# Kernel optimization log

Hardware: AMD Instinct MI355X
Metric: run time of the kernel (lower is better)

## Reference

```python
import jax, jax.numpy as jnp
import numpy as np

B, SQ, SK, D, H, DH = 4, 1024, 1024, 1024, 16, 64  # transform_units*head_units == 1024


def setup_inputs() -> dict:
    key = jax.random.key(0)
    ks = jax.random.split(key, 8)
    q = jax.random.normal(ks[0], (B, SQ, D), dtype=jnp.float32)
    v = jax.random.normal(ks[1], (B, SK, D), dtype=jnp.float32)
    q_mask = jax.random.randint(ks[2], (B, SQ), 0, 2).astype(bool).at[:, 0].set(True)
    v_mask = jax.random.randint(ks[3], (B, SK), 0, 2).astype(bool).at[:, 0].set(True)
    s = 0.02
    Wq = jax.random.normal(ks[4], (D, H * DH), dtype=jnp.float32) * s
    Wk = jax.random.normal(ks[5], (D, H * DH), dtype=jnp.float32) * s
    Wv = jax.random.normal(ks[6], (D, H * DH), dtype=jnp.float32) * s
    Wo = jax.random.normal(ks[7], (H * DH, D), dtype=jnp.float32) * s
    bq = jnp.zeros((H * DH,), jnp.float32)
    bk = jnp.zeros((H * DH,), jnp.float32)
    bv = jnp.zeros((H * DH,), jnp.float32)
    bo = jnp.zeros((D,), jnp.float32)
    return {"q": q, "v": v, "q_mask": q_mask, "v_mask": v_mask,
            "Wq": Wq, "bq": bq, "Wk": Wk, "bk": bk, "Wv": Wv, "bv": bv,
            "Wo": Wo, "bo": bo}


def reference(q, v, q_mask, v_mask, Wq, bq, Wk, bk, Wv, bv, Wo, bo):
    # k = v in the original module
    k = v
    # QKV projections; split-last-dim + batch-concat trick == reshape to heads
    Q = (q @ Wq + bq).reshape(B, SQ, H, DH)
    Kh = (k @ Wk + bk).reshape(B, SK, H, DH)
    V = (v @ Wv + bv).reshape(B, SK, H, DH)
    # Keras Attention: unscaled dot-product scores
    scores = jnp.einsum('bqhd,bkhd->bhqk', Q, Kh)  # [B,H,SQ,SK]
    scores = jnp.where(v_mask[:, None, None, :], scores, jnp.float32(-1e9))
    attn = jax.nn.softmax(scores, axis=-1)
    ctx = jnp.einsum('bhqk,bkhd->bqhd', attn, V).reshape(B, SQ, H * DH)
    # Keras Attention zeros masked query positions before output dense
    ctx = ctx * q_mask[:, :, None].astype(ctx.dtype)
    return ctx @ Wo + bo
```

## Files before the change

kernel.cpp:

```cpp
#include <hip/hip_runtime.h>
#include <hip/hip_fp16.h>

typedef __attribute__((ext_vector_type(8))) _Float16 f16x8;
typedef __attribute__((ext_vector_type(4))) float f32x4;

__device__ __forceinline__ void gload_lds16(const _Float16* g, _Float16* l) {
  __builtin_amdgcn_global_load_lds((const __attribute__((address_space(1))) void*)g,
                                   (__attribute__((address_space(3))) void*)l, 16, 0, 0);
}

__global__ __launch_bounds__(256) void cvt2_kernel(const float* __restrict__ q,
                                                   const float* __restrict__ v,
                                                   _Float16* __restrict__ q16,
                                                   _Float16* __restrict__ v16) {
  int i = blockIdx.x * 256 + threadIdx.x;
  const float* in = blockIdx.y ? v : q;
  _Float16* out = blockIdx.y ? v16 : q16;
  float4 f = ((const float4*)in)[i];
  union { _Float16 h[4]; uint2 u; } o;
  o.h[0] = (_Float16)f.x; o.h[1] = (_Float16)f.y;
  o.h[2] = (_Float16)f.z; o.h[3] = (_Float16)f.w;
  *(uint2*)&out[4 * i] = o.u;
}

__global__ __launch_bounds__(256) void transpose_cvt4_kernel(
    const float* __restrict__ W0, const float* __restrict__ W1,
    const float* __restrict__ W2, const float* __restrict__ W3,
    _Float16* __restrict__ T0, _Float16* __restrict__ T1,
    _Float16* __restrict__ T2, _Float16* __restrict__ T3) {
  int z = blockIdx.z;
  const float* W = (z == 0) ? W0 : (z == 1) ? W1 : (z == 2) ? W2 : W3;
  _Float16* T = (z == 0) ? T0 : (z == 1) ? T1 : (z == 2) ? T2 : T3;
  __shared__ float tile[64 * 65];
  int bx = blockIdx.x * 64, by = blockIdx.y * 64;
  int tid = threadIdx.x;
  for (int it = 0; it < 4; it++) {
    int lin = it * 256 + tid;
    int r = lin >> 4, q4 = (lin & 15) * 4;
    float4 f = *(const float4*)&W[(size_t)(by + r) * 1024 + bx + q4];
    tile[r * 65 + q4 + 0] = f.x;
    tile[r * 65 + q4 + 1] = f.y;
    tile[r * 65 + q4 + 2] = f.z;
    tile[r * 65 + q4 + 3] = f.w;
  }
  __syncthreads();
  for (int it = 0; it < 2; it++) {
    int lin = it * 256 + tid;
    int orow = lin >> 3, seg = (lin & 7) * 8;
    union { uint4 u; _Float16 h[8]; } o;
    for (int e = 0; e < 8; e++) o.h[e] = (_Float16)tile[(seg + e) * 65 + orow];
    *(uint4*)&T[(size_t)(bx + orow) * 1024 + by + seg] = o.u;
  }
}

__global__ __launch_bounds__(256) void transpose_v_kernel(const _Float16* __restrict__ V16,
                                                          _Float16* __restrict__ VT16) {
  __shared__ float tile[64 * 65];
  int kb = blockIdx.x, h = blockIdx.y, b = blockIdx.z;
  int tid = threadIdx.x;
  for (int it = 0; it < 2; it++) {
    int lin = it * 256 + tid;
    int r = lin >> 3, s8 = (lin & 7) * 8;
    union { uint4 u; _Float16 h[8]; } iv;
    iv.u = *(const uint4*)&V16[(size_t)(b * 1024 + kb * 64 + r) * 1024 + h * 64 + s8];
    for (int e = 0; e < 8; e++) tile[r * 65 + s8 + e] = (float)iv.h[e];
  }
  __syncthreads();
  for (int it = 0; it < 2; it++) {
    int lin = it * 256 + tid;
    int dh = lin >> 3, s8 = (lin & 7) * 8;
    union { uint4 u; _Float16 h[8]; } o;
    for (int e = 0; e < 8; e++) o.h[e] = (_Float16)tile[(s8 + e) * 65 + dh];
    *(uint4*)&VT16[((size_t)((b * 16 + h) * 64 + dh)) * 1024 + kb * 64 + s8] = o.u;
  }
}

__global__ __launch_bounds__(256) void gemm_qkv_kernel(
    const _Float16* __restrict__ q16, const _Float16* __restrict__ v16,
    const _Float16* __restrict__ WqT, const _Float16* __restrict__ WkT,
    const _Float16* __restrict__ WvT,
    const float* __restrict__ bq, const float* __restrict__ bk, const float* __restrict__ bv,
    _Float16* __restrict__ Q16, _Float16* __restrict__ K16, _Float16* __restrict__ V16) {
  int z = blockIdx.z;
  const _Float16* A = (z == 0) ? q16 : v16;
  const _Float16* BT = (z == 0) ? WqT : ((z == 1) ? WkT : WvT);
  const float* bias = (z == 0) ? bq : ((z == 1) ? bk : bv);
  _Float16* C = (z == 0) ? Q16 : ((z == 1) ? K16 : V16);
  int m0 = blockIdx.y * 128, n0 = blockIdx.x * 128;
  const int K = 1024, N = 1024;

  __shared__ _Float16 Alds[128 * 64];
  __shared__ _Float16 Blds[128 * 64];
  int tid = threadIdx.x, lane = tid & 63, w = tid >> 6;
  int c = lane & 15, g = lane >> 4;
  int wm = (w & 1) * 64, wn = (w >> 1) * 64;
  int lr = lane >> 3, ls = (lane & 7) * 8;

  const _Float16* ga[4]; const _Float16* gb[4];
  _Float16* la[4]; _Float16* lb[4];
  for (int p = 0; p < 4; p++) {
    int chunk = w * 4 + p;
    int row = chunk * 8 + lr;
    ga[p] = &A[(size_t)(m0 + row) * K + ls];
    gb[p] = &BT[(size_t)(n0 + row) * K + ls];
    la[p] = Alds + chunk * 512;
    lb[p] = Blds + chunk * 512;
  }

  f32x4 acc[4][4];
  for (int i = 0; i < 4; i++)
    for (int j = 0; j < 4; j++)
      acc[i][j] = (f32x4){0.f, 0.f, 0.f, 0.f};

  for (int kt = 0; kt < K; kt += 64) {
    __syncthreads();
    for (int p = 0; p < 4; p++) {
      gload_lds16(ga[p] + kt, la[p]);
      gload_lds16(gb[p] + kt, lb[p]);
    }
    __syncthreads();
    for (int ks = 0; ks < 2; ks++) {
      f16x8 af[4], bf[4];
      for (int i = 0; i < 4; i++)
        af[i] = *(const f16x8*)&Alds[(wm + i * 16 + c) * 64 + ks * 32 + g * 8];
      for (int j = 0; j < 4; j++)
        bf[j] = *(const f16x8*)&Blds[(wn + j * 16 + c) * 64 + ks * 32 + g * 8];
      for (int i = 0; i < 4; i++)
        for (int j = 0; j < 4; j++)
          acc[i][j] = __builtin_amdgcn_mfma_f32_16x16x32_f16(af[i], bf[j], acc[i][j], 0, 0, 0);
    }
  }
  for (int j = 0; j < 4; j++) {
    float bv_ = bias[n0 + wn + j * 16 + c];
    for (int i = 0; i < 4; i++) {
      int r = m0 + wm + i * 16 + g * 4;
      int cc = n0 + wn + j * 16 + c;
      for (int e = 0; e < 4; e++)
        C[(size_t)(r + e) * N + cc] = (_Float16)(acc[i][j][e] + bv_);
    }
  }
}

__global__ __launch_bounds__(256) void gemm_out_kernel(
    const _Float16* __restrict__ ctx16, const _Float16* __restrict__ WoT,
    const float* __restrict__ bo, float* __restrict__ out) {
  int m0 = blockIdx.y * 128, n0 = blockIdx.x * 64;
  const int K = 1024, N = 1024;
  __shared__ _Float16 Alds[128 * 64];
  __shared__ _Float16 Blds[64 * 64];
  int tid = threadIdx.x, lane = tid & 63, w = tid >> 6;
  int c = lane & 15, g = lane >> 4;
  int wm = (w & 1) * 64, wn = (w >> 1) * 32;
  int lr = lane >> 3, ls = (lane & 7) * 8;

  const _Float16* ga[4]; _Float16* la[4];
  const _Float16* gb[2]; _Float16* lb[2];
  for (int p = 0; p < 4; p++) {
    int chunk = w * 4 + p;
    int row = chunk * 8 + lr;
    ga[p] = &ctx16[(size_t)(m0 + row) * K + ls];
    la[p] = Alds + chunk * 512;
  }
  for (int p = 0; p < 2; p++) {
    int chunk = w * 2 + p;
    int row = chunk * 8 + lr;
    gb[p] = &WoT[(size_t)(n0 + row) * K + ls];
    lb[p] = Blds + chunk * 512;
  }

  f32x4 acc[4][2];
  for (int i = 0; i < 4; i++)
    for (int j = 0; j < 2; j++)
      acc[i][j] = (f32x4){0.f, 0.f, 0.f, 0.f};

  for (int kt = 0; kt < K; kt += 64) {
    __syncthreads();
    for (int p = 0; p < 4; p++) gload_lds16(ga[p] + kt, la[p]);
    for (int p = 0; p < 2; p++) gload_lds16(gb[p] + kt, lb[p]);
    __syncthreads();
    for (int ks = 0; ks < 2; ks++) {
      f16x8 af[4], bf[2];
      for (int i = 0; i < 4; i++)
        af[i] = *(const f16x8*)&Alds[(wm + i * 16 + c) * 64 + ks * 32 + g * 8];
      for (int j = 0; j < 2; j++)
        bf[j] = *(const f16x8*)&Blds[(wn + j * 16 + c) * 64 + ks * 32 + g * 8];
      for (int i = 0; i < 4; i++)
        for (int j = 0; j < 2; j++)
          acc[i][j] = __builtin_amdgcn_mfma_f32_16x16x32_f16(af[i], bf[j], acc[i][j], 0, 0, 0);
    }
  }
  for (int j = 0; j < 2; j++) {
    float bv_ = bo[n0 + wn + j * 16 + c];
    for (int i = 0; i < 4; i++) {
      int r = m0 + wm + i * 16 + g * 4;
      int cc = n0 + wn + j * 16 + c;
      for (int e = 0; e < 4; e++)
        out[(size_t)(r + e) * N + cc] = acc[i][j][e] + bv_;
    }
  }
}

__global__ __launch_bounds__(256, 4) void attn_kernel(
    const _Float16* __restrict__ Q16, const _Float16* __restrict__ K16,
    const _Float16* __restrict__ VT16,
    const int* __restrict__ q_mask, const int* __restrict__ v_mask,
    _Float16* __restrict__ ctx16) {
  int qb = blockIdx.x, h = blockIdx.y, b = blockIdx.z;
  int tid = threadIdx.x, lane = tid & 63, w = tid >> 6;
  int c = lane & 15, g = lane >> 4;
  int lr = lane >> 3, ls = lane & 7;

  __shared__ _Float16 QP[64 * 64];
  __shared__ _Float16 Kl[2][64 * 64];
  __shared__ _Float16 Vl[2][64 * 64];

  const _Float16* Qg = Q16 + ((size_t)(b * 1024 + qb * 64)) * 1024 + h * 64;
  const _Float16* Kg = K16 + ((size_t)(b * 1024)) * 1024 + h * 64;
  const _Float16* Vg = VT16 + ((size_t)(b * 16 + h)) * 64 * 1024;

  int row0 = w * 16 + lr, row1 = row0 + 8;
  int kx = (ls ^ lr) * 8;
  int ch0 = w * 2, ch1 = w * 2 + 1;

  gload_lds16(Qg + (size_t)row0 * 1024 + kx, QP + ch0 * 512);
  gload_lds16(Qg + (size_t)row1 * 1024 + kx, QP + ch1 * 512);
  gload_lds16(Kg + (size_t)row0 * 1024 + kx, &Kl[0][ch0 * 512]);
  gload_lds16(Kg + (size_t)row1 * 1024 + kx, &Kl[0][ch1 * 512]);
  gload_lds16(Vg + (size_t)row0 * 1024 + kx, &Vl[0][ch0 * 512]);
  gload_lds16(Vg + (size_t)row1 * 1024 + kx, &Vl[0][ch1 * 512]);
  __syncthreads();

  f16x8 qf[2];
  {
    int row = w * 16 + c;
    const char* rb = (const char*)QP + row * 128;
    int x = (row & 7) << 4;
    qf[0] = *(const f16x8*)(rb + ((g * 16) ^ x));
    qf[1] = *(const f16x8*)(rb + ((64 + g * 16) ^ x));
    const _Float16 l2e = (_Float16)1.44269504f;
    for (int e = 0; e < 8; e++) { qf[0][e] *= l2e; qf[1][e] *= l2e; }
  }

  float lp[4] = {0.f, 0.f, 0.f, 0.f};
  f32x4 acc_o[4];
  for (int jd = 0; jd < 4; jd++) acc_o[jd] = (f32x4){0.f, 0.f, 0.f, 0.f};

  char* pb = (char*)QP;
  int cur = 0;
  const float REF = -23.0831222f;
  for (int kb = 0; kb < 16; kb++) {
    if (kb + 1 < 16) {
      int nb = cur ^ 1;
      const _Float16* kgs = Kg + (size_t)(kb + 1) * 64 * 1024;
      const _Float16* vgs = Vg + (kb + 1) * 64;
      gload_lds16(kgs + (size_t)row0 * 1024 + kx, &Kl[nb][ch0 * 512]);
      gload_lds16(kgs + (size_t)row1 * 1024 + kx, &Kl[nb][ch1 * 512]);
      gload_lds16(vgs + (size_t)row0 * 1024 + kx, &Vl[nb][ch0 * 512]);
      gload_lds16(vgs + (size_t)row1 * 1024 + kx, &Vl[nb][ch1 * 512]);
    }
    float madd[4];
    for (int j = 0; j < 4; j++)
      madd[j] = v_mask[b * 1024 + kb * 64 + j * 16 + c] ? REF : -1e30f;

    f32x4 s[4];
    const char* kbse = (const char*)&Kl[cur][0];
    for (int j = 0; j < 4; j++) {
      int row = j * 16 + c;
      const char* rb = kbse + row * 128;
      int x = (row & 7) << 4;
      f16x8 k0 = *(const f16x8*)(rb + ((g * 16) ^ x));
      f16x8 k1 = *(const f16x8*)(rb + ((64 + g * 16) ^ x));
      s[j] = (f32x4){0.f, 0.f, 0.f, 0.f};
      s[j] = __builtin_amdgcn_mfma_f32_16x16x32_f16(qf[0], k0, s[j], 0, 0, 0);
      s[j] = __builtin_amdgcn_mfma_f32_16x16x32_f16(qf[1], k1, s[j], 0, 0, 0);
    }

    for (int j = 0; j < 4; j++)
      for (int e = 0; e < 4; e++) {
        float p = exp2f(s[j][e] + madd[j]);
        s[j][e] = p;
        lp[e] += p;
      }

    for (int j = 0; j < 4; j++)
      for (int e = 0; e < 4; e++) {
        int prow = w * 16 + g * 4 + e;
        int pby = prow * 128 + (((j * 16 + c) * 2) ^ ((prow & 7) << 4));
        *(_Float16*)(pb + pby) = (_Float16)s[j][e];
      }
    asm volatile("s_waitcnt lgkmcnt(0)" ::: "memory");
    __builtin_amdgcn_sched_barrier(0);

    const char* vbse = (const char*)&Vl[cur][0];
    for (int ks = 0; ks < 2; ks++) {
      int prow = w * 16 + c;
      f16x8 pf = *(const f16x8*)(pb + prow * 128 +
                                 ((ks * 64 + g * 16) ^ ((prow & 7) << 4)));
      for (int jd = 0; jd < 4; jd++) {
        int vrow = jd * 16 + c;
        f16x8 vf = *(const f16x8*)(vbse + vrow * 128 +
                                   ((ks * 64 + g * 16) ^ ((vrow & 7) << 4)));
        acc_o[jd] = __builtin_amdgcn_mfma_f32_16x16x32_f16(pf, vf, acc_o[jd], 0, 0, 0);
      }
    }

    __syncthreads();
    cur ^= 1;
  }

  for (int e = 0; e < 4; e++) {
    lp[e] += __shfl_xor(lp[e], 1);
    lp[e] += __shfl_xor(lp[e], 2);
    lp[e] += __shfl_xor(lp[e], 4);
    lp[e] += __shfl_xor(lp[e], 8);
  }

  int qrow = b * 1024 + qb * 64 + w * 16 + g * 4;
  float inv[4];
  for (int e = 0; e < 4; e++) {
    float qm = q_mask[qrow + e] ? 1.0f : 0.0f;
    inv[e] = qm / lp[e];
  }
  _Float16* cb = ctx16 + ((size_t)qrow) * 1024 + h * 64;
  for (int jd = 0; jd < 4; jd++)
    for (int e = 0; e < 4; e++)
      cb[(size_t)e * 1024 + jd * 16 + c] = (_Float16)(acc_o[jd][e] * inv[e]);
}

extern "C" void kernel_launch(void* const* d_in, const int* in_sizes, int n_in,
                              void* d_out, int out_size, void* d_ws, size_t ws_size,
                              hipStream_t stream) {
  const float* q  = (const float*)d_in[0];
  const float* v  = (const float*)d_in[1];
  const int* q_mask = (const int*)d_in[2];
  const int* v_mask = (const int*)d_in[3];
  const float* Wq = (const float*)d_in[4];
  const float* bq = (const float*)d_in[5];
  const float* Wk = (const float*)d_in[6];
  const float* bk = (const float*)d_in[7];
  const float* Wv = (const float*)d_in[8];
  const float* bv = (const float*)d_in[9];
  const float* Wo = (const float*)d_in[10];
  const float* bo = (const float*)d_in[11];
  float* out = (float*)d_out;

  _Float16* ws = (_Float16*)d_ws;
  const size_t NE = (size_t)4 * 1024 * 1024;
  _Float16* q16   = ws;
  _Float16* v16   = ws + NE;
  _Float16* Q16   = ws + 2 * NE;
  _Float16* K16   = ws + 3 * NE;
  _Float16* V16   = ws + 4 * NE;
  _Float16* ctx16 = ws + 5 * NE;
  _Float16* WqT   = ws + 6 * NE;
  _Float16* WkT   = WqT + 1024 * 1024;
  _Float16* WvT   = WkT + 1024 * 1024;
  _Float16* WoT   = WvT + 1024 * 1024;
  _Float16* VT16  = q16;

  cvt2_kernel<<<dim3(4096, 2), 256, 0, stream>>>(q, v, q16, v16);
  transpose_cvt4_kernel<<<dim3(16, 16, 4), 256, 0, stream>>>(Wq, Wk, Wv, Wo, WqT, WkT, WvT, WoT);
  gemm_qkv_kernel<<<dim3(8, 32, 3), 256, 0, stream>>>(q16, v16, WqT, WkT, WvT,
                                                      bq, bk, bv, Q16, K16, V16);
  transpose_v_kernel<<<dim3(16, 16, 4), 256, 0, stream>>>(V16, VT16);
  attn_kernel<<<dim3(16, 16, 4), 256, 0, stream>>>(Q16, K16, VT16, q_mask, v_mask, ctx16);
  gemm_out_kernel<<<dim3(16, 32), 256, 0, stream>>>(ctx16, WoT, bo, out);
}
```

Measured before the change: 224.3 us.

## Double-buffer GEMM LDS tiles with XOR swizzle, fuse prep and V transpose

Both GEMM kernels now double-buffer their LDS tiles. Each iteration prefetches the next K tile with global_load_lds while MFMAs run on the current one, with a single barrier per iteration. Loads and reads use an XOR swizzle on the 16-byte column chunk to cut LDS bank conflicts. The fp16 conversion and weight transpose kernels merge into one launch, and the V projection epilogue writes V transposed per head directly, removing the separate transpose kernel and its round trip through global memory. The costs are doubled LDS use, which may lower occupancy, and scattered 8-byte stores in the V epilogue.

Result: no change. 221.9 us (-1.0%).

```diff
diff --git a/kernel.cpp b/kernel.cpp
--- a/kernel.cpp
+++ b/kernel.cpp
@@ -9,31 +9,32 @@
                                    (__attribute__((address_space(3))) void*)l, 16, 0, 0);
 }
 
-__global__ __launch_bounds__(256) void cvt2_kernel(const float* __restrict__ q,
-                                                   const float* __restrict__ v,
-                                                   _Float16* __restrict__ q16,
-                                                   _Float16* __restrict__ v16) {
-  int i = blockIdx.x * 256 + threadIdx.x;
-  const float* in = blockIdx.y ? v : q;
-  _Float16* out = blockIdx.y ? v16 : q16;
-  float4 f = ((const float4*)in)[i];
-  union { _Float16 h[4]; uint2 u; } o;
-  o.h[0] = (_Float16)f.x; o.h[1] = (_Float16)f.y;
-  o.h[2] = (_Float16)f.z; o.h[3] = (_Float16)f.w;
-  *(uint2*)&out[4 * i] = o.u;
-}
-
-__global__ __launch_bounds__(256) void transpose_cvt4_kernel(
+__global__ __launch_bounds__(256) void prep_kernel(
+    const float* __restrict__ q, const float* __restrict__ v,
     const float* __restrict__ W0, const float* __restrict__ W1,
     const float* __restrict__ W2, const float* __restrict__ W3,
+    _Float16* __restrict__ q16, _Float16* __restrict__ v16,
     _Float16* __restrict__ T0, _Float16* __restrict__ T1,
     _Float16* __restrict__ T2, _Float16* __restrict__ T3) {
-  int z = blockIdx.z;
+  __shared__ float tile[64 * 65];
+  int tid = threadIdx.x, ybl = blockIdx.y;
+  if (ybl < 16) {
+    int i = (ybl * 256 + blockIdx.x) * 256 + tid;
+    float4 fq = ((const float4*)q)[i];
+    float4 fv = ((const float4*)v)[i];
+    union { _Float16 h[4]; uint2 u; } oq, ov;
+    oq.h[0] = (_Float16)fq.x; oq.h[1] = (_Float16)fq.y;
+    oq.h[2] = (_Float16)fq.z; oq.h[3] = (_Float16)fq.w;
+    ov.h[0] = (_Float16)fv.x; ov.h[1] = (_Float16)fv.y;
+    ov.h[2] = (_Float16)fv.z; ov.h[3] = (_Float16)fv.w;
+    *(uint2*)&q16[4 * (size_t)i] = oq.u;
+    *(uint2*)&v16[4 * (size_t)i] = ov.u;
+    return;
+  }
+  int z = ybl - 16;
   const float* W = (z == 0) ? W0 : (z == 1) ? W1 : (z == 2) ? W2 : W3;
   _Float16* T = (z == 0) ? T0 : (z == 1) ? T1 : (z == 2) ? T2 : T3;
-  __shared__ float tile[64 * 65];
-  int bx = blockIdx.x * 64, by = blockIdx.y * 64;
-  int tid = threadIdx.x;
+  int bx = (blockIdx.x & 15) * 64, by = (blockIdx.x >> 4) * 64;
   for (int it = 0; it < 4; it++) {
     int lin = it * 256 + tid;
     int r = lin >> 4, q4 = (lin & 15) * 4;
@@ -53,58 +54,35 @@
   }
 }
 
-__global__ __launch_bounds__(256) void transpose_v_kernel(const _Float16* __restrict__ V16,
-                                                          _Float16* __restrict__ VT16) {
-  __shared__ float tile[64 * 65];
-  int kb = blockIdx.x, h = blockIdx.y, b = blockIdx.z;
-  int tid = threadIdx.x;
-  for (int it = 0; it < 2; it++) {
-    int lin = it * 256 + tid;
-    int r = lin >> 3, s8 = (lin & 7) * 8;
-    union { uint4 u; _Float16 h[8]; } iv;
-    iv.u = *(const uint4*)&V16[(size_t)(b * 1024 + kb * 64 + r) * 1024 + h * 64 + s8];
-    for (int e = 0; e < 8; e++) tile[r * 65 + s8 + e] = (float)iv.h[e];
-  }
-  __syncthreads();
-  for (int it = 0; it < 2; it++) {
-    int lin = it * 256 + tid;
-    int dh = lin >> 3, s8 = (lin & 7) * 8;
-    union { uint4 u; _Float16 h[8]; } o;
-    for (int e = 0; e < 8; e++) o.h[e] = (_Float16)tile[(s8 + e) * 65 + dh];
-    *(uint4*)&VT16[((size_t)((b * 16 + h) * 64 + dh)) * 1024 + kb * 64 + s8] = o.u;
-  }
-}
-
 __global__ __launch_bounds__(256) void gemm_qkv_kernel(
     const _Float16* __restrict__ q16, const _Float16* __restrict__ v16,
     const _Float16* __restrict__ WqT, const _Float16* __restrict__ WkT,
     const _Float16* __restrict__ WvT,
     const float* __restrict__ bq, const float* __restrict__ bk, const float* __restrict__ bv,
-    _Float16* __restrict__ Q16, _Float16* __restrict__ K16, _Float16* __restrict__ V16) {
+    _Float16* __restrict__ Q16, _Float16* __restrict__ K16, _Float16* __restrict__ VT16) {
   int z = blockIdx.z;
   const _Float16* A = (z == 0) ? q16 : v16;
   const _Float16* BT = (z == 0) ? WqT : ((z == 1) ? WkT : WvT);
   const float* bias = (z == 0) ? bq : ((z == 1) ? bk : bv);
-  _Float16* C = (z == 0) ? Q16 : ((z == 1) ? K16 : V16);
   int m0 = blockIdx.y * 128, n0 = blockIdx.x * 128;
-  const int K = 1024, N = 1024;
-
-  __shared__ _Float16 Alds[128 * 64];
-  __shared__ _Float16 Blds[128 * 64];
+  const int K = 1024;
+
+  __shared__ _Float16 Alds[2][128 * 64];
+  __shared__ _Float16 Blds[2][128 * 64];
   int tid = threadIdx.x, lane = tid & 63, w = tid >> 6;
   int c = lane & 15, g = lane >> 4;
   int wm = (w & 1) * 64, wn = (w >> 1) * 64;
-  int lr = lane >> 3, ls = (lane & 7) * 8;
+  int lr = lane >> 3;
+  int ls = ((lane & 7) ^ lr) * 8;
 
   const _Float16* ga[4]; const _Float16* gb[4];
-  _Float16* la[4]; _Float16* lb[4];
+  int loff[4];
   for (int p = 0; p < 4; p++) {
     int chunk = w * 4 + p;
     int row = chunk * 8 + lr;
     ga[p] = &A[(size_t)(m0 + row) * K + ls];
     gb[p] = &BT[(size_t)(n0 + row) * K + ls];
-    la[p] = Alds + chunk * 512;
-    lb[p] = Blds + chunk * 512;
+    loff[p] = chunk * 512;
   }
 
   f32x4 acc[4][4];
@@ -112,31 +90,61 @@
     for (int j = 0; j < 4; j++)
       acc[i][j] = (f32x4){0.f, 0.f, 0.f, 0.f};
 
-  for (int kt = 0; kt < K; kt += 64) {
-    __syncthreads();
-    for (int p = 0; p < 4; p++) {
-      gload_lds16(ga[p] + kt, la[p]);
-      gload_lds16(gb[p] + kt, lb[p]);
-    }
-    __syncthreads();
+  for (int p = 0; p < 4; p++) {
+    gload_lds16(ga[p], &Alds[0][loff[p]]);
+    gload_lds16(gb[p], &Blds[0][loff[p]]);
+  }
+  __syncthreads();
+
+  int xa = (c & 7) << 4;
+  int cur = 0;
+  for (int kt = 0; kt < 16; kt++) {
+    if (kt + 1 < 16) {
+      int nb = cur ^ 1;
+      for (int p = 0; p < 4; p++) {
+        gload_lds16(ga[p] + (kt + 1) * 64, &Alds[nb][loff[p]]);
+        gload_lds16(gb[p] + (kt + 1) * 64, &Blds[nb][loff[p]]);
+      }
+    }
+    const char* ab = (const char*)&Alds[cur][0];
+    const char* bb = (const char*)&Blds[cur][0];
     for (int ks = 0; ks < 2; ks++) {
       f16x8 af[4], bf[4];
       for (int i = 0; i < 4; i++)
-        af[i] = *(const f16x8*)&Alds[(wm + i * 16 + c) * 64 + ks * 32 + g * 8];
+        af[i] = *(const f16x8*)(ab + (wm + i * 16 + c) * 128 + ((ks * 64 + g * 16) ^ xa));
       for (int j = 0; j < 4; j++)
-        bf[j] = *(const f16x8*)&Blds[(wn + j * 16 + c) * 64 + ks * 32 + g * 8];
+        bf[j] = *(const f16x8*)(bb + (wn + j * 16 + c) * 128 + ((ks * 64 + g * 16) ^ xa));
       for (int i = 0; i < 4; i++)
         for (int j = 0; j < 4; j++)
           acc[i][j] = __builtin_amdgcn_mfma_f32_16x16x32_f16(af[i], bf[j], acc[i][j], 0, 0, 0);
     }
-  }
-  for (int j = 0; j < 4; j++) {
-    float bv_ = bias[n0 + wn + j * 16 + c];
-    for (int i = 0; i < 4; i++) {
-      int r = m0 + wm + i * 16 + g * 4;
+    __syncthreads();
+    cur ^= 1;
+  }
+
+  if (z < 2) {
+    _Float16* C = (z == 0) ? Q16 : K16;
+    for (int j = 0; j < 4; j++) {
+      float bv_ = bias[n0 + wn + j * 16 + c];
+      for (int i = 0; i < 4; i++) {
+        int r = m0 + wm + i * 16 + g * 4;
+        int cc = n0 + wn + j * 16 + c;
+        for (int e = 0; e < 4; e++)
+          C[(size_t)(r + e) * 1024 + cc] = (_Float16)(acc[i][j][e] + bv_);
+      }
+    }
+  } else {
+    for (int j = 0; j < 4; j++) {
       int cc = n0 + wn + j * 16 + c;
-      for (int e = 0; e < 4; e++)
-        C[(size_t)(r + e) * N + cc] = (_Float16)(acc[i][j][e] + bv_);
+      float bv_ = bias[cc];
+      int h_ = cc >> 6, dh = cc & 63;
+      for (int i = 0; i < 4; i++) {
+        int r = m0 + wm + i * 16 + g * 4;
+        int b_ = r >> 10, key = r & 1023;
+        union { uint2 u; _Float16 hh[4]; } o;
+        for (int e = 0; e < 4; e++) o.hh[e] = (_Float16)(acc[i][j][e] + bv_);
+        *(uint2*)&VT16[((size_t)((b_ * 16 + h_) * 64 + dh)) * 1024 + key] = o.u;
+      }
     }
   }
 }
@@ -145,27 +153,28 @@
     const _Float16* __restrict__ ctx16, const _Float16* __restrict__ WoT,
     const float* __restrict__ bo, float* __restrict__ out) {
   int m0 = blockIdx.y * 128, n0 = blockIdx.x * 64;
-  const int K = 1024, N = 1024;
-  __shared__ _Float16 Alds[128 * 64];
-  __shared__ _Float16 Blds[64 * 64];
+  const int K = 1024;
+  __shared__ _Float16 Alds[2][128 * 64];
+  __shared__ _Float16 Blds[2][64 * 64];
   int tid = threadIdx.x, lane = tid & 63, w = tid >> 6;
   int c = lane & 15, g = lane >> 4;
   int wm = (w & 1) * 64, wn = (w >> 1) * 32;
-  int lr = lane >> 3, ls = (lane & 7) * 8;
-
-  const _Float16* ga[4]; _Float16* la[4];
-  const _Float16* gb[2]; _Float16* lb[2];
+  int lr = lane >> 3;
+  int ls = ((lane & 7) ^ lr) * 8;
+
+  const _Float16* ga[4]; int laoff[4];
+  const _Float16* gb[2]; int lboff[2];
   for (int p = 0; p < 4; p++) {
     int chunk = w * 4 + p;
     int row = chunk * 8 + lr;
     ga[p] = &ctx16[(size_t)(m0 + row) * K + ls];
-    la[p] = Alds + chunk * 512;
+    laoff[p] = chunk * 512;
   }
   for (int p = 0; p < 2; p++) {
     int chunk = w * 2 + p;
     int row = chunk * 8 + lr;
     gb[p] = &WoT[(size_t)(n0 + row) * K + ls];
-    lb[p] = Blds + chunk * 512;
+    lboff[p] = chunk * 512;
   }
 
   f32x4 acc[4][2];
@@ -173,21 +182,32 @@
     for (int j = 0; j < 2; j++)
       acc[i][j] = (f32x4){0.f, 0.f, 0.f, 0.f};
 
-  for (int kt = 0; kt < K; kt += 64) {
-    __syncthreads();
-    for (int p = 0; p < 4; p++) gload_lds16(ga[p] + kt, la[p]);
-    for (int p = 0; p < 2; p++) gload_lds16(gb[p] + kt, lb[p]);
-    __syncthreads();
+  for (int p = 0; p < 4; p++) gload_lds16(ga[p], &Alds[0][laoff[p]]);
+  for (int p = 0; p < 2; p++) gload_lds16(gb[p], &Blds[0][lboff[p]]);
+  __syncthreads();
+
+  int xa = (c & 7) << 4;
+  int cur = 0;
+  for (int kt = 0; kt < 16; kt++) {
+    if (kt + 1 < 16) {
+      int nb = cur ^ 1;
+      for (int p = 0; p < 4; p++) gload_lds16(ga[p] + (kt + 1) * 64, &Alds[nb][laoff[p]]);
+      for (int p = 0; p < 2; p++) gload_lds16(gb[p] + (kt + 1) * 64, &Blds[nb][lboff[p]]);
+    }
+    const char* ab = (const char*)&Alds[cur][0];
+    const char* bb = (const char*)&Blds[cur][0];
     for (int ks = 0; ks < 2; ks++) {
       f16x8 af[4], bf[2];
       for (int i = 0; i < 4; i++)
-        af[i] = *(const f16x8*)&Alds[(wm + i * 16 + c) * 64 + ks * 32 + g * 8];
+        af[i] = *(const f16x8*)(ab + (wm + i * 16 + c) * 128 + ((ks * 64 + g * 16) ^ xa));
       for (int j = 0; j < 2; j++)
-        bf[j] = *(const f16x8*)&Blds[(wn + j * 16 + c) * 64 + ks * 32 + g * 8];
+        bf[j] = *(const f16x8*)(bb + (wn + j * 16 + c) * 128 + ((ks * 64 + g * 16) ^ xa));
       for (int i = 0; i < 4; i++)
         for (int j = 0; j < 2; j++)
           acc[i][j] = __builtin_amdgcn_mfma_f32_16x16x32_f16(af[i], bf[j], acc[i][j], 0, 0, 0);
     }
+    __syncthreads();
+    cur ^= 1;
   }
   for (int j = 0; j < 2; j++) {
     float bv_ = bo[n0 + wn + j * 16 + c];
@@ -195,7 +215,7 @@
       int r = m0 + wm + i * 16 + g * 4;
       int cc = n0 + wn + j * 16 + c;
       for (int e = 0; e < 4; e++)
-        out[(size_t)(r + e) * N + cc] = acc[i][j][e] + bv_;
+        out[(size_t)(r + e) * 1024 + cc] = acc[i][j][e] + bv_;
     }
   }
 }
@@ -350,19 +370,17 @@
   _Float16* v16   = ws + NE;
   _Float16* Q16   = ws + 2 * NE;
   _Float16* K16   = ws + 3 * NE;
-  _Float16* V16   = ws + 4 * NE;
+  _Float16* VT16  = ws + 4 * NE;
   _Float16* ctx16 = ws + 5 * NE;
   _Float16* WqT   = ws + 6 * NE;
   _Float16* WkT   = WqT + 1024 * 1024;
   _Float16* WvT   = WkT + 1024 * 1024;
   _Float16* WoT   = WvT + 1024 * 1024;
-  _Float16* VT16  = q16;
-
-  cvt2_kernel<<<dim3(4096, 2), 256, 0, stream>>>(q, v, q16, v16);
-  transpose_cvt4_kernel<<<dim3(16, 16, 4), 256, 0, stream>>>(Wq, Wk, Wv, Wo, WqT, WkT, WvT, WoT);
+
+  prep_kernel<<<dim3(256, 20), 256, 0, stream>>>(q, v, Wq, Wk, Wv, Wo,
+                                                 q16, v16, WqT, WkT, WvT, WoT);
   gemm_qkv_kernel<<<dim3(8, 32, 3), 256, 0, stream>>>(q16, v16, WqT, WkT, WvT,
-                                                      bq, bk, bv, Q16, K16, V16);
-  transpose_v_kernel<<<dim3(16, 16, 4), 256, 0, stream>>>(V16, VT16);
+                                                      bq, bk, bv, Q16, K16, VT16);
   attn_kernel<<<dim3(16, 16, 4), 256, 0, stream>>>(Q16, K16, VT16, q_mask, v_mask, ctx16);
   gemm_out_kernel<<<dim3(16, 32), 256, 0, stream>>>(ctx16, WoT, bo, out);
 }
```
